# Kernel optimization log

Measured on AMD Instinct MI355X. Metric: run time of the kernel, lower is better.

## Reference

```python
import math
import jax, jax.numpy as jnp
import numpy as np

B, T, C, H = 4, 2048, 1024, 16
HD = C // H

def gelu_tanh(x):
    return 0.5 * x * (1.0 + jnp.tanh(jnp.sqrt(2.0 / jnp.pi) * (x + 0.044715 * x * x * x)))

def layernorm(x, w, b, eps=1e-5):
    mu = jnp.mean(x, axis=-1, keepdims=True)
    var = jnp.var(x, axis=-1, keepdims=True)
    return (x - mu) * jax.lax.rsqrt(var + eps) * w + b

def setup_inputs() -> dict:
    key = jax.random.key(0)
    ks = jax.random.split(key, 8)
    s = 0.02
    return {
        "x": jax.random.normal(ks[0], (B, T, C), dtype=jnp.float32),
        "ln1_w": jnp.ones((C,), jnp.float32), "ln1_b": jnp.zeros((C,), jnp.float32),
        "attn_w": jax.random.normal(ks[1], (C, 3 * C), jnp.float32) * s,
        "attn_b": jnp.zeros((3 * C,), jnp.float32),
        "proj_w": jax.random.normal(ks[2], (C, C), jnp.float32) * s,
        "proj_b": jnp.zeros((C,), jnp.float32),
        "ln2_w": jnp.ones((C,), jnp.float32), "ln2_b": jnp.zeros((C,), jnp.float32),
        "fc_w": jax.random.normal(ks[3], (C, 4 * C), jnp.float32) * s,
        "fc_b": jnp.zeros((4 * C,), jnp.float32),
        "fc_proj_w": jax.random.normal(ks[4], (4 * C, C), jnp.float32) * s,
        "fc_proj_b": jnp.zeros((C,), jnp.float32),
    }

def block(x, ln1_w, ln1_b, attn_w, attn_b, proj_w, proj_b,
          ln2_w, ln2_b, fc_w, fc_b, fc_proj_w, fc_proj_b):
    # --- causal self-attention ---
    h = layernorm(x, ln1_w, ln1_b)
    qkv = h @ attn_w + attn_b                      # [B,T,3C]
    q, k, v = jnp.split(qkv, 3, axis=-1)
    q = q.reshape(B, T, H, HD).transpose(0, 2, 1, 3)  # [B,H,T,hd]
    k = k.reshape(B, T, H, HD).transpose(0, 2, 1, 3)
    v = v.reshape(B, T, H, HD).transpose(0, 2, 1, 3)
    att = jnp.einsum('bhqd,bhkd->bhqk', q, k) * (1.0 / math.sqrt(HD))
    mask = jnp.tril(jnp.ones((T, T), dtype=bool))
    att = jnp.where(mask, att, -jnp.inf)
    att = jax.nn.softmax(att, axis=-1)
    y = jnp.einsum('bhqk,bhkd->bhqd', att, v)
    y = y.transpose(0, 2, 1, 3).reshape(B, T, C)
    x = x + (y @ proj_w + proj_b)
    # --- MLP ---
    h = layernorm(x, ln2_w, ln2_b)
    h = gelu_tanh(h @ fc_w + fc_b)
    x = x + (h @ fc_proj_w + fc_proj_b)
    return x

def reference(x, ln1_w, ln1_b, attn_w, attn_b, proj_w, proj_b,
              ln2_w, ln2_b, fc_w, fc_b, fc_proj_w, fc_proj_b):
    return block(x, ln1_w, ln1_b, attn_w, attn_b, proj_w, proj_b,
                 ln2_w, ln2_b, fc_w, fc_b, fc_proj_w, fc_proj_b)
```

## Files before the change

### kernel.cpp

```cpp
#include <hip/hip_runtime.h>
#include <stdint.h>

#define TSEQ 2048
#define CDIM 1024
#define NHEAD 16
#define HDIM 64
#define NROWS 8192

typedef __bf16 bf16x8 __attribute__((ext_vector_type(8)));
typedef float f32x4 __attribute__((ext_vector_type(4)));
typedef float f32x16 __attribute__((ext_vector_type(16)));

__device__ __forceinline__ unsigned short f2bf(float f) {
  unsigned u = __builtin_bit_cast(unsigned, f);
  u = u + 0x7fffu + ((u >> 16) & 1u);
  return (unsigned short)(u >> 16);
}

__device__ __forceinline__ unsigned cvt_pk_bf16(float a, float b) {
  unsigned r;
  asm("v_cvt_pk_bf16_f32 %0, %1, %2" : "=v"(r) : "v"(a), "v"(b));
  return r;
}

__device__ __forceinline__ float gelu_f(float x) {
  float x3 = x * x * x;
  float z = 0.7978845608028654f * (x + 0.044715f * x3);
  float e = __expf(2.f * z);
  float t = 1.f - 2.f / (e + 1.f);
  return 0.5f * x * (1.f + t);
}

__device__ __forceinline__ void ldg_lds16(void* lds, const void* gsrc) {
  __builtin_amdgcn_global_load_lds(
      (__attribute__((address_space(1))) unsigned int*)(uintptr_t)gsrc,
      (__attribute__((address_space(3))) unsigned int*)lds,
      16, 0, 0);
}

__global__ __launch_bounds__(256) void k_wtrans(const float* __restrict__ W,
                                                unsigned short* __restrict__ Wt,
                                                int K, int N) {
  __shared__ unsigned short tl[32][40];
  int n0 = blockIdx.x * 32, k0 = blockIdx.y * 32;
  int tid = threadIdx.x;
  int r = tid >> 3, c4 = (tid & 7) * 4;
  float4 v = *(const float4*)(W + (size_t)(k0 + r) * N + n0 + c4);
  ushort4 o;
  o.x = f2bf(v.x); o.y = f2bf(v.y); o.z = f2bf(v.z); o.w = f2bf(v.w);
  *(ushort4*)&tl[r][c4] = o;
  __syncthreads();
  int n = tid >> 3, k4 = (tid & 7) * 4;
  ushort4 w;
  w.x = tl[k4 + 0][n]; w.y = tl[k4 + 1][n]; w.z = tl[k4 + 2][n]; w.w = tl[k4 + 3][n];
  *(ushort4*)(Wt + (size_t)(n0 + n) * K + k0 + k4) = w;
}

__global__ __launch_bounds__(256) void k_ln(const float* __restrict__ x,
                                            const float* __restrict__ w,
                                            const float* __restrict__ b,
                                            unsigned short* __restrict__ out) {
  int row = blockIdx.x;
  int tid = threadIdx.x;
  const float* xr = x + (size_t)row * CDIM;
  float4 v = *(const float4*)(xr + tid * 4);
  float s = v.x + v.y + v.z + v.w;
  float s2 = v.x * v.x + v.y * v.y + v.z * v.z + v.w * v.w;
#pragma unroll
  for (int off = 32; off; off >>= 1) {
    s += __shfl_xor(s, off);
    s2 += __shfl_xor(s2, off);
  }
  __shared__ float rbuf[8];
  int wv = tid >> 6, lane = tid & 63;
  if (lane == 0) { rbuf[wv] = s; rbuf[4 + wv] = s2; }
  __syncthreads();
  float S1 = rbuf[0] + rbuf[1] + rbuf[2] + rbuf[3];
  float S2 = rbuf[4] + rbuf[5] + rbuf[6] + rbuf[7];
  float mean = S1 * (1.f / CDIM);
  float var = S2 * (1.f / CDIM) - mean * mean;
  float rstd = rsqrtf(var + 1e-5f);
  float4 wv4 = *(const float4*)(w + tid * 4);
  float4 bv4 = *(const float4*)(b + tid * 4);
  ushort4 o;
  o.x = f2bf((v.x - mean) * rstd * wv4.x + bv4.x);
  o.y = f2bf((v.y - mean) * rstd * wv4.y + bv4.y);
  o.z = f2bf((v.z - mean) * rstd * wv4.z + bv4.z);
  o.w = f2bf((v.w - mean) * rstd * wv4.w + bv4.w);
  *(ushort4*)(out + (size_t)row * CDIM + tid * 4) = o;
}

template <int EPI>
__global__ __launch_bounds__(512, 2)
void k_gemm8(const unsigned short* __restrict__ A,
             const unsigned short* __restrict__ Bt,
             const float* __restrict__ bias,
             const float* __restrict__ resid,
             void* __restrict__ Cout,
             int M, int N, int K) {
  __shared__ __align__(16) unsigned short lds[3 * 24576];
  const int tid = threadIdx.x;
  const int wid = tid >> 6, lane = tid & 63;
  const int wm = wid >> 2, wn = wid & 3;
  const int fr = lane & 15, fq = lane >> 4;

  const int gx = gridDim.x;
  int flat = blockIdx.y * gx + blockIdx.x;
  {
    const int nwg = gx * gridDim.y;
    int q = nwg >> 3, r = nwg & 7;
    int xcd = flat & 7, idx = flat >> 3;
    flat = (xcd < r ? xcd * (q + 1) : r * (q + 1) + (xcd - r) * q) + idx;
  }
  const int bx = flat % gx, by = flat / gx;
  const long brow = (long)by * 128, bcol = (long)bx * 256;

  const int lrow = lane >> 3;
  const int kby = ((lane & 7) << 4) ^ (((lane >> 5) & 1) << 5);
  const char* gA = (const char*)(A + ((size_t)(brow + wid * 16 + lrow)) * K) + kby;
  const char* gB = (const char*)(Bt + ((size_t)(bcol + wid * 32 + lrow)) * K) + kby;

  const int NT = K >> 6;

#define STAGE_A(i, t, bf_)                                              \
  ldg_lds16((char*)(lds + (bf_) * 24576) + (wid * 2 + (i)) * 1024,      \
            gA + ((size_t)(i) * 8 * K + (size_t)(t) * 64) * 2)
#define STAGE_B(j, t, bf_)                                              \
  ldg_lds16((char*)(lds + (bf_) * 24576 + 8192) + (wid * 4 + (j)) * 1024, \
            gB + ((size_t)(j) * 8 * K + (size_t)(t) * 64) * 2)

  STAGE_A(0, 0, 0); STAGE_A(1, 0, 0);
  STAGE_B(0, 0, 0); STAGE_B(1, 0, 0); STAGE_B(2, 0, 0); STAGE_B(3, 0, 0);
  STAGE_A(0, 1, 1); STAGE_A(1, 1, 1);
  STAGE_B(0, 1, 1); STAGE_B(1, 1, 1); STAGE_B(2, 1, 1); STAGE_B(3, 1, 1);

  f32x4 acc[4][4];
  const f32x4 vzero = {0.f, 0.f, 0.f, 0.f};
#pragma unroll
  for (int m = 0; m < 4; ++m)
#pragma unroll
    for (int n = 0; n < 4; ++n) acc[m][n] = vzero;

  const int swz = (fq << 4) ^ ((fr & 4) << 3);
  int buf = 0;
  for (int t = 0; t < NT; ++t) {
    if (t + 1 < NT) asm volatile("s_waitcnt vmcnt(6)" ::: "memory");
    else            asm volatile("s_waitcnt vmcnt(0)" ::: "memory");
    __builtin_amdgcn_s_barrier();
    __builtin_amdgcn_sched_barrier(0);
    const char* pA = (const char*)(lds + buf * 24576);
    const char* pB = pA + 16384;
    int nbuf = buf + 2; if (nbuf >= 3) nbuf -= 3;
    if (t + 2 < NT) { STAGE_A(0, t + 2, nbuf); STAGE_A(1, t + 2, nbuf); STAGE_B(0, t + 2, nbuf); }
    bf16x8 bfrag[4][2];
#pragma unroll
    for (int n = 0; n < 4; ++n)
#pragma unroll
      for (int kh = 0; kh < 2; ++kh)
        bfrag[n][kh] = *(const bf16x8*)(pB + (wn * 64 + n * 16 + fr) * 128 + kh * 64 + swz);
    bf16x8 af01[2][2];
#pragma unroll
    for (int m = 0; m < 2; ++m)
#pragma unroll
      for (int kh = 0; kh < 2; ++kh)
        af01[m][kh] = *(const bf16x8*)(pA + (wm * 64 + m * 16 + fr) * 128 + kh * 64 + swz);
    __builtin_amdgcn_s_setprio(1);
#pragma unroll
    for (int m = 0; m < 2; ++m)
#pragma unroll
      for (int n = 0; n < 4; ++n)
#pragma unroll
        for (int kh = 0; kh < 2; ++kh)
          acc[m][n] = __builtin_amdgcn_mfma_f32_16x16x32_bf16(af01[m][kh], bfrag[n][kh], acc[m][n], 0, 0, 0);
    __builtin_amdgcn_s_setprio(0);
    __builtin_amdgcn_s_barrier();
    if (t + 2 < NT) { STAGE_B(1, t + 2, nbuf); STAGE_B(2, t + 2, nbuf); STAGE_B(3, t + 2, nbuf); }
    bf16x8 af23[2][2];
#pragma unroll
    for (int m = 0; m < 2; ++m)
#pragma unroll
      for (int kh = 0; kh < 2; ++kh)
        af23[m][kh] = *(const bf16x8*)(pA + (wm * 64 + (m + 2) * 16 + fr) * 128 + kh * 64 + swz);
    __builtin_amdgcn_s_setprio(1);
#pragma unroll
    for (int m = 0; m < 2; ++m)
#pragma unroll
      for (int n = 0; n < 4; ++n)
#pragma unroll
        for (int kh = 0; kh < 2; ++kh)
          acc[m + 2][n] = __builtin_amdgcn_mfma_f32_16x16x32_bf16(af23[m][kh], bfrag[n][kh], acc[m + 2][n], 0, 0, 0);
    __builtin_amdgcn_s_setprio(0);
    buf = buf + 1; if (buf == 3) buf = 0;
  }
#undef STAGE_A
#undef STAGE_B

#pragma unroll
  for (int m = 0; m < 4; ++m) {
    long row = brow + wm * 64 + m * 16 + fq * 4;
#pragma unroll
    for (int n = 0; n < 4; ++n) {
      long col = bcol + wn * 64 + n * 16 + fr;
      float bv = bias[col];
#pragma unroll
      for (int r = 0; r < 4; ++r) {
        float v = acc[m][n][r] + bv;
        long idx = (row + r) * (long)N + col;
        if (EPI == 0) {
          ((unsigned short*)Cout)[idx] = f2bf(v);
        } else if (EPI == 1) {
          ((unsigned short*)Cout)[idx] = f2bf(gelu_f(v));
        } else {
          ((float*)Cout)[idx] = v + resid[idx];
        }
      }
    }
  }
}

__global__ __launch_bounds__(256) void k_build_vt(const unsigned short* __restrict__ qkv,
                                                  unsigned short* __restrict__ vt) {
  __shared__ __align__(16) unsigned short tl[64][80];
  int bh = blockIdx.x, b = bh >> 4, h = bh & 15;
  int t0 = blockIdx.y * 64;
  int tid = threadIdx.x;
  int r = tid >> 2, cb = (tid & 3) * 16;
  const unsigned short* src =
      qkv + (size_t)(b * TSEQ + t0 + r) * (3 * CDIM) + 2 * CDIM + h * HDIM + cb;
  *(uint4*)&tl[r][cb] = *(const uint4*)src;
  *(uint4*)&tl[r][cb + 8] = *(const uint4*)(src + 8);
  __syncthreads();
  int d = tid >> 2, tb = (tid & 3) * 16;
  union { unsigned short u[16]; uint4 v[2]; } o;
#pragma unroll
  for (int j = 0; j < 16; ++j) o.u[j] = tl[tb + j][d];
  unsigned short* dst = vt + ((size_t)bh * HDIM + d) * TSEQ + t0 + tb;
  *(uint4*)dst = o.v[0];
  *(uint4*)(dst + 8) = o.v[1];
}

struct QSt {
  f32x16 OTlo, OThi;
  float m, l;
};

__device__ __forceinline__ void attn_qk_sm_pv(
    const bf16x8& k0, const bf16x8& k1, const bf16x8& k2, const bf16x8& k3,
    const bf16x8& v0, const bf16x8& v1, const bf16x8& v2, const bf16x8& v3,
    const bf16x8& q0f, const bf16x8& q1f, const bf16x8& q2f, const bf16x8& q3f,
    QSt& S, bool diag, int lq, int hi) {
  const float SC = 0.125f * 1.44269504088896f;
  f32x16 st;
#pragma unroll
  for (int r = 0; r < 16; ++r) st[r] = 0.f;
  st = __builtin_amdgcn_mfma_f32_32x32x16_bf16(k0, q0f, st, 0, 0, 0);
  st = __builtin_amdgcn_mfma_f32_32x32x16_bf16(k1, q1f, st, 0, 0, 0);
  st = __builtin_amdgcn_mfma_f32_32x32x16_bf16(k2, q2f, st, 0, 0, 0);
  st = __builtin_amdgcn_mfma_f32_32x32x16_bf16(k3, q3f, st, 0, 0, 0);
#pragma unroll
  for (int r = 0; r < 16; ++r) st[r] *= SC;
  if (diag) {
#pragma unroll
    for (int r = 0; r < 16; ++r) {
      int kvl = (r & 3) + 8 * (r >> 2) + 4 * hi;
      if (kvl > lq) st[r] = -1e30f;
    }
  }
  float tmax = st[0];
#pragma unroll
  for (int r = 1; r < 16; ++r) tmax = fmaxf(tmax, st[r]);
  float tm = fmaxf(tmax, __shfl_xor(tmax, 32));
  if (__any(tm > S.m + 8.f)) {
    float mnew = fmaxf(S.m, tm);
    float alpha = __builtin_amdgcn_exp2f(S.m - mnew);
    S.m = mnew;
    S.OTlo *= alpha;
    S.OThi *= alpha;
    S.l *= alpha;
  }
  unsigned c[8];
  float rs = 0.f;
#pragma unroll
  for (int i = 0; i < 8; ++i) {
    float pa = __builtin_amdgcn_exp2f(st[2 * i] - S.m);
    float pb = __builtin_amdgcn_exp2f(st[2 * i + 1] - S.m);
    rs += pa + pb;
    c[i] = cvt_pk_bf16(pa, pb);
  }
  S.l += rs + __shfl_xor(rs, 32);
  unsigned pc[8];
#pragma unroll
  for (int i = 0; i < 8; ++i) pc[i] = __shfl_xor(c[i], 32);
  uint4 w1, w2;
  w1.x = hi ? pc[2] : c[0]; w1.y = hi ? pc[3] : c[1];
  w1.z = hi ? c[2] : pc[0]; w1.w = hi ? c[3] : pc[1];
  w2.x = hi ? pc[6] : c[4]; w2.y = hi ? pc[7] : c[5];
  w2.z = hi ? c[6] : pc[4]; w2.w = hi ? c[7] : pc[5];
  bf16x8 f1 = __builtin_bit_cast(bf16x8, w1);
  bf16x8 f2 = __builtin_bit_cast(bf16x8, w2);
  S.OTlo = __builtin_amdgcn_mfma_f32_32x32x16_bf16(v0, f1, S.OTlo, 0, 0, 0);
  S.OTlo = __builtin_amdgcn_mfma_f32_32x32x16_bf16(v1, f2, S.OTlo, 0, 0, 0);
  S.OThi = __builtin_amdgcn_mfma_f32_32x32x16_bf16(v2, f1, S.OThi, 0, 0, 0);
  S.OThi = __builtin_amdgcn_mfma_f32_32x32x16_bf16(v3, f2, S.OThi, 0, 0, 0);
}

__global__ __launch_bounds__(256, 2) void k_attn(const unsigned short* __restrict__ qkv,
                                                 const unsigned short* __restrict__ vt,
                                                 unsigned short* __restrict__ y) {
  const int bh = blockIdx.x, b = bh >> 4, h = bh & 15;
  const int wv = threadIdx.x >> 6, lane = threadIdx.x & 63;
  const int w = blockIdx.y * 4 + wv;
  const int lq = lane & 31, hi = lane >> 5;
  const int ntL = w, ntH = 63 - w;
  const int q0L = w * 32, q0H = (63 - w) * 32;

  const unsigned short* qrowL = qkv + ((size_t)(b * TSEQ) + q0L + lq) * (3 * CDIM) + h * HDIM;
  const unsigned short* qrowH = qkv + ((size_t)(b * TSEQ) + q0H + lq) * (3 * CDIM) + h * HDIM;
  bf16x8 qL0 = *(const bf16x8*)(qrowL + 0 + hi * 8);
  bf16x8 qL1 = *(const bf16x8*)(qrowL + 16 + hi * 8);
  bf16x8 qL2 = *(const bf16x8*)(qrowL + 32 + hi * 8);
  bf16x8 qL3 = *(const bf16x8*)(qrowL + 48 + hi * 8);
  bf16x8 qH0 = *(const bf16x8*)(qrowH + 0 + hi * 8);
  bf16x8 qH1 = *(const bf16x8*)(qrowH + 16 + hi * 8);
  bf16x8 qH2 = *(const bf16x8*)(qrowH + 32 + hi * 8);
  bf16x8 qH3 = *(const bf16x8*)(qrowH + 48 + hi * 8);

  const unsigned short* kbase = qkv + ((size_t)(b * TSEQ) + lq) * (3 * CDIM) + CDIM + h * HDIM;
  const unsigned short* vbase = vt + ((size_t)bh * HDIM + lq) * TSEQ;

  QSt SL, SH;
#pragma unroll
  for (int r = 0; r < 16; ++r) {
    SL.OTlo[r] = 0.f; SL.OThi[r] = 0.f; SH.OTlo[r] = 0.f; SH.OThi[r] = 0.f;
  }
  SL.m = -1e30f; SL.l = 0.f; SH.m = -1e30f; SH.l = 0.f;

#define LOADKV(K0_, K1_, K2_, K3_, V0_, V1_, V2_, V3_, tt)                 \
  do {                                                                     \
    const unsigned short* kr_ = kbase + (size_t)(tt) * 32 * (3 * CDIM);    \
    K0_ = *(const bf16x8*)(kr_ + 0 + hi * 8);                              \
    K1_ = *(const bf16x8*)(kr_ + 16 + hi * 8);                             \
    K2_ = *(const bf16x8*)(kr_ + 32 + hi * 8);                             \
    K3_ = *(const bf16x8*)(kr_ + 48 + hi * 8);                             \
    const unsigned short* vr_ = vbase + (tt) * 32;                         \
    V0_ = *(const bf16x8*)(vr_ + hi * 8);                                  \
    V1_ = *(const bf16x8*)(vr_ + 16 + hi * 8);                             \
    V2_ = *(const bf16x8*)(vr_ + 32 * TSEQ + hi * 8);                      \
    V3_ = *(const bf16x8*)(vr_ + 32 * TSEQ + 16 + hi * 8);                 \
  } while (0)

  bf16x8 kA0, kA1, kA2, kA3, vA0, vA1, vA2, vA3;
  bf16x8 kB0, kB1, kB2, kB3, vB0, vB1, vB2, vB3;
  LOADKV(kA0, kA1, kA2, kA3, vA0, vA1, vA2, vA3, 0);
  for (int t = 0;; t += 2) {
    if (t + 1 <= ntH) LOADKV(kB0, kB1, kB2, kB3, vB0, vB1, vB2, vB3, t + 1);
    attn_qk_sm_pv(kA0, kA1, kA2, kA3, vA0, vA1, vA2, vA3,
                  qH0, qH1, qH2, qH3, SH, t == ntH, lq, hi);
    if (t <= ntL)
      attn_qk_sm_pv(kA0, kA1, kA2, kA3, vA0, vA1, vA2, vA3,
                    qL0, qL1, qL2, qL3, SL, t == ntL, lq, hi);
    if (t + 1 > ntH) break;
    if (t + 2 <= ntH) LOADKV(kA0, kA1, kA2, kA3, vA0, vA1, vA2, vA3, t + 2);
    attn_qk_sm_pv(kB0, kB1, kB2, kB3, vB0, vB1, vB2, vB3,
                  qH0, qH1, qH2, qH3, SH, t + 1 == ntH, lq, hi);
    if (t + 1 <= ntL)
      attn_qk_sm_pv(kB0, kB1, kB2, kB3, vB0, vB1, vB2, vB3,
                    qL0, qL1, qL2, qL3, SL, t + 1 == ntL, lq, hi);
    if (t + 2 > ntH) break;
  }
#undef LOADKV

  {
    float inv = 1.f / SH.l;
    unsigned short* yrow = y + ((size_t)(b * TSEQ) + q0H + lq) * CDIM + h * HDIM;
#pragma unroll
    for (int r = 0; r < 16; r += 2) {
      int d = (r & 3) + 8 * (r >> 2) + 4 * hi;
      unsigned lo0 = f2bf(SH.OTlo[r] * inv), lo1 = f2bf(SH.OTlo[r + 1] * inv);
      *(unsigned*)(yrow + d) = lo0 | (lo1 << 16);
      unsigned h0 = f2bf(SH.OThi[r] * inv), h1 = f2bf(SH.OThi[r + 1] * inv);
      *(unsigned*)(yrow + 32 + d) = h0 | (h1 << 16);
    }
  }
  {
    float inv = 1.f / SL.l;
    unsigned short* yrow = y + ((size_t)(b * TSEQ) + q0L + lq) * CDIM + h * HDIM;
#pragma unroll
    for (int r = 0; r < 16; r += 2) {
      int d = (r & 3) + 8 * (r >> 2) + 4 * hi;
      unsigned lo0 = f2bf(SL.OTlo[r] * inv), lo1 = f2bf(SL.OTlo[r + 1] * inv);
      *(unsigned*)(yrow + d) = lo0 | (lo1 << 16);
      unsigned h0 = f2bf(SL.OThi[r] * inv), h1 = f2bf(SL.OThi[r + 1] * inv);
      *(unsigned*)(yrow + 32 + d) = h0 | (h1 << 16);
    }
  }
}

extern "C" void kernel_launch(void* const* d_in, const int* in_sizes, int n_in,
                              void* d_out, int out_size, void* d_ws, size_t ws_size,
                              hipStream_t stream) {
  const float* x = (const float*)d_in[0];
  const float* ln1_w = (const float*)d_in[1];
  const float* ln1_b = (const float*)d_in[2];
  const float* attn_w = (const float*)d_in[3];
  const float* attn_b = (const float*)d_in[4];
  const float* proj_w = (const float*)d_in[5];
  const float* proj_b = (const float*)d_in[6];
  const float* ln2_w = (const float*)d_in[7];
  const float* ln2_b = (const float*)d_in[8];
  const float* fc_w = (const float*)d_in[9];
  const float* fc_b = (const float*)d_in[10];
  const float* fc_proj_w = (const float*)d_in[11];
  const float* fc_proj_b = (const float*)d_in[12];

  char* ws = (char*)d_ws;
  unsigned short* wt_attn = (unsigned short*)(ws + 0);
  unsigned short* wt_proj = (unsigned short*)(ws + 6291456);
  unsigned short* wt_fc = (unsigned short*)(ws + 8388608);
  unsigned short* wt_fcp = (unsigned short*)(ws + 16777216);
  float* x1 = (float*)(ws + 25165824);
  unsigned short* hbuf = (unsigned short*)(ws + 58720256);
  unsigned short* ybuf = (unsigned short*)(ws + 75497472);
  unsigned short* qkvb = (unsigned short*)(ws + 92274688);
  unsigned short* vtb = (unsigned short*)(ws + 142606336);
  unsigned short* gbuf = (unsigned short*)(ws + 92274688);

  k_wtrans<<<dim3(3072 / 32, 1024 / 32), 256, 0, stream>>>(attn_w, wt_attn, 1024, 3072);
  k_wtrans<<<dim3(1024 / 32, 1024 / 32), 256, 0, stream>>>(proj_w, wt_proj, 1024, 1024);
  k_wtrans<<<dim3(4096 / 32, 1024 / 32), 256, 0, stream>>>(fc_w, wt_fc, 1024, 4096);
  k_wtrans<<<dim3(1024 / 32, 4096 / 32), 256, 0, stream>>>(fc_proj_w, wt_fcp, 4096, 1024);

  k_ln<<<NROWS, 256, 0, stream>>>(x, ln1_w, ln1_b, hbuf);

  k_gemm8<0><<<dim3(3072 / 256, NROWS / 128), 512, 0, stream>>>(
      hbuf, wt_attn, attn_b, nullptr, qkvb, NROWS, 3072, 1024);

  k_build_vt<<<dim3(64, TSEQ / 64), 256, 0, stream>>>(qkvb, vtb);

  k_attn<<<dim3(64, 8), 256, 0, stream>>>(qkvb, vtb, ybuf);

  k_gemm8<2><<<dim3(1024 / 256, NROWS / 128), 512, 0, stream>>>(
      ybuf, wt_proj, proj_b, x, x1, NROWS, 1024, 1024);

  k_ln<<<NROWS, 256, 0, stream>>>(x1, ln2_w, ln2_b, hbuf);

  k_gemm8<1><<<dim3(4096 / 256, NROWS / 128), 512, 0, stream>>>(
      hbuf, wt_fc, fc_b, nullptr, gbuf, NROWS, 4096, 1024);

  k_gemm8<2><<<dim3(1024 / 256, NROWS / 128), 512, 0, stream>>>(
      gbuf, wt_fcp, fc_proj_b, x1, (float*)d_out, NROWS, 1024, 4096);
}
```

Measured before the change: 417.3 us.

## Stage K/V tiles in shared memory via direct global-to-LDS loads in attention

The attention kernel now has the four waves of a block cooperatively load each 32-key K/V tile into a double-buffered LDS area using global-to-LDS loads, instead of each wave loading its own copy into registers. Waves then read their fragments from LDS. This cuts redundant global/L2 traffic by roughly a factor of four and frees the registers that held the double-buffered K/V fragments. The cost is a block-wide barrier every tile, and waves with shorter causal ranges now wait on the block's longest wave.

```diff
diff --git a/kernel.cpp b/kernel.cpp
--- a/kernel.cpp
+++ b/kernel.cpp
@@ -307,12 +307,16 @@
 __global__ __launch_bounds__(256, 2) void k_attn(const unsigned short* __restrict__ qkv,
                                                  const unsigned short* __restrict__ vt,
                                                  unsigned short* __restrict__ y) {
+  __shared__ __align__(16) unsigned short Ks[2][2048];
+  __shared__ __align__(16) unsigned short Vs[2][2048];
   const int bh = blockIdx.x, b = bh >> 4, h = bh & 15;
   const int wv = threadIdx.x >> 6, lane = threadIdx.x & 63;
-  const int w = blockIdx.y * 4 + wv;
+  const int by = blockIdx.y;
+  const int w = by * 4 + wv;
   const int lq = lane & 31, hi = lane >> 5;
   const int ntL = w, ntH = 63 - w;
   const int q0L = w * 32, q0H = (63 - w) * 32;
+  const int T = 64 - 4 * by;
 
   const unsigned short* qrowL = qkv + ((size_t)(b * TSEQ) + q0L + lq) * (3 * CDIM) + h * HDIM;
   const unsigned short* qrowH = qkv + ((size_t)(b * TSEQ) + q0H + lq) * (3 * CDIM) + h * HDIM;
@@ -325,8 +329,16 @@
   bf16x8 qH2 = *(const bf16x8*)(qrowH + 32 + hi * 8);
   bf16x8 qH3 = *(const bf16x8*)(qrowH + 48 + hi * 8);
 
-  const unsigned short* kbase = qkv + ((size_t)(b * TSEQ) + lq) * (3 * CDIM) + CDIM + h * HDIM;
-  const unsigned short* vbase = vt + ((size_t)bh * HDIM + lq) * TSEQ;
+  const int kr = lane & 31, kc = wv * 2 + (lane >> 5);
+  const unsigned short* gK =
+      qkv + ((size_t)(b * TSEQ) + kr) * (3 * CDIM) + CDIM + h * HDIM + kc * 8;
+  const unsigned short* gV = vt + ((size_t)bh * HDIM + lane) * TSEQ + wv * 8;
+
+#define STAGEKV(bf_, tt)                                                  \
+  do {                                                                    \
+    ldg_lds16((char*)Ks[bf_] + wv * 1024, gK + (size_t)(tt) * 32 * (3 * CDIM)); \
+    ldg_lds16((char*)Vs[bf_] + wv * 1024, gV + (tt) * 32);                \
+  } while (0)
 
   QSt SL, SH;
 #pragma unroll
@@ -335,40 +347,29 @@
   }
   SL.m = -1e30f; SL.l = 0.f; SH.m = -1e30f; SH.l = 0.f;
 
-#define LOADKV(K0_, K1_, K2_, K3_, V0_, V1_, V2_, V3_, tt)                 \
-  do {                                                                     \
-    const unsigned short* kr_ = kbase + (size_t)(tt) * 32 * (3 * CDIM);    \
-    K0_ = *(const bf16x8*)(kr_ + 0 + hi * 8);                              \
-    K1_ = *(const bf16x8*)(kr_ + 16 + hi * 8);                             \
-    K2_ = *(const bf16x8*)(kr_ + 32 + hi * 8);                             \
-    K3_ = *(const bf16x8*)(kr_ + 48 + hi * 8);                             \
-    const unsigned short* vr_ = vbase + (tt) * 32;                         \
-    V0_ = *(const bf16x8*)(vr_ + hi * 8);                                  \
-    V1_ = *(const bf16x8*)(vr_ + 16 + hi * 8);                             \
-    V2_ = *(const bf16x8*)(vr_ + 32 * TSEQ + hi * 8);                      \
-    V3_ = *(const bf16x8*)(vr_ + 32 * TSEQ + 16 + hi * 8);                 \
-  } while (0)
-
-  bf16x8 kA0, kA1, kA2, kA3, vA0, vA1, vA2, vA3;
-  bf16x8 kB0, kB1, kB2, kB3, vB0, vB1, vB2, vB3;
-  LOADKV(kA0, kA1, kA2, kA3, vA0, vA1, vA2, vA3, 0);
-  for (int t = 0;; t += 2) {
-    if (t + 1 <= ntH) LOADKV(kB0, kB1, kB2, kB3, vB0, vB1, vB2, vB3, t + 1);
-    attn_qk_sm_pv(kA0, kA1, kA2, kA3, vA0, vA1, vA2, vA3,
-                  qH0, qH1, qH2, qH3, SH, t == ntH, lq, hi);
-    if (t <= ntL)
-      attn_qk_sm_pv(kA0, kA1, kA2, kA3, vA0, vA1, vA2, vA3,
-                    qL0, qL1, qL2, qL3, SL, t == ntL, lq, hi);
-    if (t + 1 > ntH) break;
-    if (t + 2 <= ntH) LOADKV(kA0, kA1, kA2, kA3, vA0, vA1, vA2, vA3, t + 2);
-    attn_qk_sm_pv(kB0, kB1, kB2, kB3, vB0, vB1, vB2, vB3,
-                  qH0, qH1, qH2, qH3, SH, t + 1 == ntH, lq, hi);
-    if (t + 1 <= ntL)
-      attn_qk_sm_pv(kB0, kB1, kB2, kB3, vB0, vB1, vB2, vB3,
-                    qL0, qL1, qL2, qL3, SL, t + 1 == ntL, lq, hi);
-    if (t + 2 > ntH) break;
-  }
-#undef LOADKV
+  STAGEKV(0, 0);
+  for (int t = 0; t < T; ++t) {
+    __syncthreads();
+    if (t + 1 < T) STAGEKV((t + 1) & 1, t + 1);
+    if (t <= ntH) {
+      const unsigned short* Kb = Ks[t & 1];
+      const unsigned short* Vb = Vs[t & 1];
+      bf16x8 k0 = *(const bf16x8*)(Kb + (0 + hi) * 256 + lq * 8);
+      bf16x8 k1 = *(const bf16x8*)(Kb + (2 + hi) * 256 + lq * 8);
+      bf16x8 k2 = *(const bf16x8*)(Kb + (4 + hi) * 256 + lq * 8);
+      bf16x8 k3 = *(const bf16x8*)(Kb + (6 + hi) * 256 + lq * 8);
+      bf16x8 v0 = *(const bf16x8*)(Vb + hi * 512 + lq * 8);
+      bf16x8 v1 = *(const bf16x8*)(Vb + (2 + hi) * 512 + lq * 8);
+      bf16x8 v2 = *(const bf16x8*)(Vb + hi * 512 + (lq + 32) * 8);
+      bf16x8 v3 = *(const bf16x8*)(Vb + (2 + hi) * 512 + (lq + 32) * 8);
+      attn_qk_sm_pv(k0, k1, k2, k3, v0, v1, v2, v3,
+                    qH0, qH1, qH2, qH3, SH, t == ntH, lq, hi);
+      if (t <= ntL)
+        attn_qk_sm_pv(k0, k1, k2, k3, v0, v1, v2, v3,
+                      qL0, qL1, qL2, qL3, SL, t == ntL, lq, hi);
+    }
+  }
+#undef STAGEKV
 
   {
     float inv = 1.f / SH.l;
```

New measurement: 390.2 us. 1.07x faster.
